# Kernel optimization log

Hardware: AMD Instinct MI355X
Metric: run time of the kernel (lower is better)

## Reference

```python
import jax, jax.numpy as jnp
import numpy as np

B, T, W = 4, 2048, 1024
K, G = 7, 8            # kernel_size, groups
Cg = W // G            # channels per group
SE_R = 16              # SE reduction ratio
LN_EPS = 1e-5


def setup_inputs() -> dict:
    key = jax.random.key(0)
    ks = jax.random.split(key, 8)
    h = jax.random.normal(ks[0], (B, T, W), jnp.float32)
    # mask: True = padding; valid prefix of random length per row
    lengths = jax.random.randint(ks[1], (B,), T // 2, T + 1)
    mask = jnp.arange(T)[None, :] >= lengths[:, None]
    s_w = np.float32(1.0 / np.sqrt(W))
    return dict(
        h=h,
        mask=mask,
        offset_w=jax.random.normal(ks[2], (W, K), jnp.float32) * 0.01,
        offset_b=jnp.zeros((K,), jnp.float32),
        conv_w=jax.random.normal(ks[3], (G, Cg, Cg, K), jnp.float32) * np.float32(1.0 / np.sqrt(Cg * K)),
        conv_b=jnp.zeros((W,), jnp.float32),
        ln_g=jnp.ones((W,), jnp.float32),
        ln_b=jnp.zeros((W,), jnp.float32),
        se_w1=jax.random.normal(ks[4], (W, W // SE_R), jnp.float32) * s_w,
        se_b1=jnp.zeros((W // SE_R,), jnp.float32),
        se_w2=jax.random.normal(ks[5], (W // SE_R, W), jnp.float32) * np.float32(1.0 / np.sqrt(W // SE_R)),
        se_b2=jnp.zeros((W,), jnp.float32),
        proj_w=jax.random.normal(ks[6], (W, 1), jnp.float32) * s_w,
        proj_b=jnp.zeros((1,), jnp.float32),
    )


def deform_conv1d(h, offset_w, offset_b, conv_w, conv_b):
    # h: [B,T,W]. Learned per-(position, tap) fractional offsets; linear interp gather;
    # grouped conv combine. conv_w: [G, out_per_group, in_per_group, K].
    Bn, Tn, Wn = h.shape
    pad = (K - 1) // 2
    offsets = h @ offset_w + offset_b                                   # [B,T,K]
    base = (jnp.arange(Tn, dtype=jnp.float32)[None, :, None]
            + (jnp.arange(K, dtype=jnp.float32) - pad)[None, None, :])  # [1,T,K]
    pos = jnp.clip(base + offsets, 0.0, Tn - 1.0)                       # [B,T,K]
    p0 = jnp.floor(pos).astype(jnp.int32)
    p1 = jnp.minimum(p0 + 1, Tn - 1)
    frac = (pos - p0.astype(jnp.float32))[..., None]                    # [B,T,K,1]
    gather = jax.vmap(lambda hb, ib: hb[ib])                            # [T,W],[T,K] -> [T,K,W]
    sampled = gather(h, p0) * (1.0 - frac) + gather(h, p1) * frac       # [B,T,K,W]
    sg = sampled.reshape(Bn, Tn, K, G, Cg)
    out = jnp.einsum('btkgc,gock->btgo', sg, conv_w).reshape(Bn, Tn, Wn)
    return out + conv_b


def layer_norm(x, g, b):
    mu = jnp.mean(x, axis=-1, keepdims=True)
    var = jnp.mean(jnp.square(x - mu), axis=-1, keepdims=True)
    return (x - mu) * jax.lax.rsqrt(var + LN_EPS) * g + b


def se_block(x, mask, w1, b1, w2, b2):
    valid = (~mask).astype(x.dtype)[..., None]                          # [B,T,1]
    lengths = jnp.clip(jnp.sum(valid, axis=1), 1.0)                     # [B,1]
    s = jnp.sum(x * valid, axis=1) / lengths                            # [B,W]
    gate = jax.nn.sigmoid(jax.nn.relu(s @ w1 + b1) @ w2 + b2)           # [B,W]
    return x * gate[:, None, :]


def reference(h, mask, offset_w, offset_b, conv_w, conv_b, ln_g, ln_b,
              se_w1, se_b1, se_w2, se_b2, proj_w, proj_b):
    x = layer_norm(deform_conv1d(h, offset_w, offset_b, conv_w, conv_b), ln_g, ln_b)
    x = se_block(x, mask, se_w1, se_b1, se_w2, se_b2)
    # dropout: identity in eval mode (p handled outside reference)
    valid = (~mask).astype(x.dtype)[..., None]
    x = x * valid                                                       # masked_fill(mask, 0)
    lengths = jnp.clip(jnp.sum(valid, axis=1), 1.0)                     # [B,1]
    pooled = jnp.sum(x, axis=1) / lengths                               # [B,W]
    return jnp.squeeze(pooled @ proj_w + proj_b, axis=-1)               # [B]
```

## Files before the change

kernel.cpp:

```cpp
#include <hip/hip_runtime.h>
#include <hip/hip_bf16.h>

#define Bdim 4
#define Tdim 2048
#define Wdim 1024
#define Kdim 7
#define Gdim 8
#define Cg   128
#define Hdim 64
#define TT   64

typedef __attribute__((ext_vector_type(8))) short short8v;
typedef __attribute__((ext_vector_type(4))) float float4v;

__device__ __forceinline__ short f2bf(float x) {
    union { float f; unsigned u; } v; v.f = x;
    unsigned r = v.u + 0x7fff + ((v.u >> 16) & 1);
    return (short)(r >> 16);
}

__device__ __forceinline__ unsigned pack2bf(float lo, float hi) {
    return __builtin_amdgcn_perm(__float_as_uint(hi) + 0x8000u,
                                 __float_as_uint(lo) + 0x8000u, 0x07060302u);
}

__device__ __forceinline__ short8v lerp_pack(uint4 a, uint4 b, float f) {
    union { uint4 u; short8v s; } r;
    const unsigned* pa = (const unsigned*)&a;
    const unsigned* pb = (const unsigned*)&b;
    unsigned* pr = (unsigned*)&r.u;
#pragma unroll
    for (int d = 0; d < 4; d++) {
        float alo = __uint_as_float(pa[d] << 16);
        float ahi = __uint_as_float(pa[d] & 0xffff0000u);
        float blo = __uint_as_float(pb[d] << 16);
        float bhi = __uint_as_float(pb[d] & 0xffff0000u);
        float rlo = alo + f * (blo - alo);
        float rhi = ahi + f * (bhi - ahi);
        pr[d] = pack2bf(rlo, rhi);
    }
    return r.s;
}

__global__ __launch_bounds__(256) void k_pre(const float* __restrict__ conv_w,
                                             short* __restrict__ Wtb,
                                             const float* __restrict__ h,
                                             const float* __restrict__ offset_w,
                                             const float* __restrict__ offset_b,
                                             float* __restrict__ pos,
                                             ushort* __restrict__ h16,
                                             float* __restrict__ rowstat) {
    int tid = threadIdx.x;
    if (blockIdx.x < 448) {
        if (blockIdx.x < 64) rowstat[blockIdx.x * 256 + tid] = 0.f;
        int i = blockIdx.x * 256 + tid;
        int cb = i & 15;
        int o = (i >> 4) & 127;
        int gk = i >> 11;
        int k = gk % Kdim, g = gk / Kdim;
        const float* src = conv_w + ((size_t)(g * Cg + o) * Cg + cb * 8) * Kdim + k;
        short8v pk;
#pragma unroll
        for (int j = 0; j < 8; j++) pk[j] = f2bf(src[(size_t)j * Kdim]);
        short8v* Wtb8 = (short8v*)Wtb;
        Wtb8[(size_t)gk * 2048 + o * 16 + cb] = pk;
        return;
    }
    int lane = tid & 63, wv = tid >> 6;
    int bt = (blockIdx.x - 448) * 4 + wv;
    int t = bt & (Tdim - 1);
    const float* row = h + (size_t)bt * Wdim;
    float acc[Kdim];
#pragma unroll
    for (int k = 0; k < Kdim; k++) acc[k] = 0.f;
#pragma unroll
    for (int j = 0; j < 4; j++) {
        int c = lane * 4 + j * 256;
        float4 hv = *(const float4*)(row + c);
        const float* ow = offset_w + (size_t)c * Kdim;
#pragma unroll
        for (int k = 0; k < Kdim; k++)
            acc[k] += hv.x * ow[k] + hv.y * ow[Kdim + k] + hv.z * ow[2 * Kdim + k]
                    + hv.w * ow[3 * Kdim + k];
        ushort4 hp;
        hp.x = (ushort)f2bf(hv.x); hp.y = (ushort)f2bf(hv.y);
        hp.z = (ushort)f2bf(hv.z); hp.w = (ushort)f2bf(hv.w);
        *(ushort4*)(h16 + (size_t)bt * Wdim + c) = hp;
    }
#pragma unroll
    for (int k = 0; k < Kdim; k++) {
#pragma unroll
        for (int m = 32; m > 0; m >>= 1) acc[k] += __shfl_xor(acc[k], m);
    }
    if (lane < Kdim) {
        float o = acc[lane] + offset_b[lane];
        float base = (float)t + (float)(lane - 3);
        float p = fminf(fmaxf(base + o, 0.f), (float)(Tdim - 1));
        pos[bt * Kdim + lane] = p;
    }
}

__global__ __launch_bounds__(256, 3) void k_conv(const ushort* __restrict__ h16,
                                                 const short* __restrict__ Wtb,
                                                 const float* __restrict__ conv_b,
                                                 const float* __restrict__ pos,
                                                 ushort* __restrict__ y16,
                                                 float* __restrict__ rowstat) {
    __shared__ short8v sA8[2][TT * 16];
    __shared__ float posl[TT * 8];

    int blk = blockIdx.x;
    int g  = blk & 7;
    int tc = (blk >> 3) & 31;
    int b  = blk >> 8;
    int t0 = tc * TT;
    int tid = threadIdx.x;
    int lane = tid & 63, wv = tid >> 6;
    int r15 = lane & 15, q = lane >> 4;

    const ushort* hb = h16 + (size_t)(b * Tdim) * Wdim + g * Cg;
    const short8v* WtbV = (const short8v*)Wtb + (size_t)(g * Kdim) * 2048;

    int scb = tid & 15;
    int sr0 = tid >> 4;

    {
        int base = (b * Tdim + t0) * Kdim;
        for (int u = tid; u < TT * Kdim; u += 256) {
            int r = u / 7, kk = u - r * 7;
            posl[r * 8 + kk] = pos[base + u];
        }
    }
    __syncthreads();

    float4v acc[4][2];
#pragma unroll
    for (int tt = 0; tt < 4; tt++)
#pragma unroll
        for (int n = 0; n < 2; n++) acc[tt][n] = (float4v){0.f, 0.f, 0.f, 0.f};

    float fr[4];
    uint4 glo[4], ghi[4];
    short8v bfr[8];

#pragma unroll
    for (int i = 0; i < 4; i++) {
        int r = sr0 + i * 16;
        float p = posl[r * 8 + 0];
        int p0 = (int)p;
        fr[i] = p - (float)p0;
        int p1 = min(p0 + 1, Tdim - 1);
        glo[i] = *(const uint4*)(hb + (size_t)p0 * Wdim + scb * 8);
        ghi[i] = *(const uint4*)(hb + (size_t)p1 * Wdim + scb * 8);
    }
#pragma unroll
    for (int n = 0; n < 2; n++)
#pragma unroll
        for (int kk = 0; kk < 4; kk++)
            bfr[n * 4 + kk] = WtbV[(wv * 32 + n * 16 + r15) * 16 + kk * 4 + q];
#pragma unroll
    for (int i = 0; i < 4; i++) {
        int r = sr0 + i * 16;
        sA8[0][r * 16 + (scb ^ (r & 7))] = lerp_pack(glo[i], ghi[i], fr[i]);
    }
    asm volatile("s_waitcnt lgkmcnt(0)" ::: "memory");
    __builtin_amdgcn_s_barrier();
    asm volatile("" ::: "memory");

#pragma unroll 1
    for (int k = 0; k < Kdim; k++) {
        int cur = k & 1;
        short8v* buf = sA8[cur];
        if (k < Kdim - 1) {
#pragma unroll
            for (int i = 0; i < 4; i++) {
                int r = sr0 + i * 16;
                float p = posl[r * 8 + k + 1];
                int p0 = (int)p;
                fr[i] = p - (float)p0;
                int p1 = min(p0 + 1, Tdim - 1);
                glo[i] = *(const uint4*)(hb + (size_t)p0 * Wdim + scb * 8);
                ghi[i] = *(const uint4*)(hb + (size_t)p1 * Wdim + scb * 8);
            }
        }
#pragma unroll
        for (int tt = 0; tt < 4; tt++) {
            int r = tt * 16 + r15;
            short8v af[4];
#pragma unroll
            for (int kk = 0; kk < 4; kk++)
                af[kk] = buf[r * 16 + ((kk * 4 + q) ^ (r & 7))];
#pragma unroll
            for (int kk = 0; kk < 4; kk++) {
#pragma unroll
                for (int n = 0; n < 2; n++)
                    acc[tt][n] = __builtin_amdgcn_mfma_f32_16x16x32_bf16(
                        af[kk], bfr[n * 4 + kk], acc[tt][n], 0, 0, 0);
            }
        }
        if (k < Kdim - 1) {
            short8v* nbuf = sA8[cur ^ 1];
#pragma unroll
            for (int i = 0; i < 4; i++) {
                int r = sr0 + i * 16;
                nbuf[r * 16 + (scb ^ (r & 7))] = lerp_pack(glo[i], ghi[i], fr[i]);
            }
#pragma unroll
            for (int n = 0; n < 2; n++)
#pragma unroll
                for (int kk = 0; kk < 4; kk++)
                    bfr[n * 4 + kk] =
                        WtbV[(size_t)(k + 1) * 2048 + (wv * 32 + n * 16 + r15) * 16 + kk * 4 + q];
            asm volatile("s_waitcnt lgkmcnt(0)" ::: "memory");
            __builtin_amdgcn_s_barrier();
            asm volatile("" ::: "memory");
        }
    }
    __syncthreads();
    float* ep = (float*)sA8;
#pragma unroll
    for (int n = 0; n < 2; n++) {
        int colb = wv * 32 + n * 16 + r15;
        float bias = conv_b[g * Cg + colb];
#pragma unroll
        for (int tt = 0; tt < 4; tt++)
#pragma unroll
            for (int j = 0; j < 4; j++) {
                int row = tt * 16 + q * 4 + j;
                ep[row * 128 + (colb ^ ((row & 7) << 2))] = acc[tt][n][j] + bias;
            }
    }
    __syncthreads();
    int row = tid >> 2, c0 = (tid & 3) * 32;
    int sw = (row & 7) << 2;
    ushort* yp = y16 + (size_t)(b * Tdim + t0 + row) * Wdim + g * Cg + c0;
    float s_part = 0.f, q_part = 0.f;
#pragma unroll
    for (int s = 0; s < 4; s++) {
        float4 va = *(const float4*)&ep[row * 128 + ((c0 + s * 8) ^ sw)];
        float4 vb = *(const float4*)&ep[row * 128 + ((c0 + s * 8 + 4) ^ sw)];
        s_part += va.x + va.y + va.z + va.w + vb.x + vb.y + vb.z + vb.w;
        q_part += va.x * va.x + va.y * va.y + va.z * va.z + va.w * va.w
                + vb.x * vb.x + vb.y * vb.y + vb.z * vb.z + vb.w * vb.w;
        uint4 o;
        o.x = pack2bf(va.x, va.y);
        o.y = pack2bf(va.z, va.w);
        o.z = pack2bf(vb.x, vb.y);
        o.w = pack2bf(vb.z, vb.w);
        *(uint4*)(yp + s * 8) = o;
    }
    s_part += __shfl_xor(s_part, 1); s_part += __shfl_xor(s_part, 2);
    q_part += __shfl_xor(q_part, 1); q_part += __shfl_xor(q_part, 2);
    if ((tid & 3) == 0) {
        atomicAdd(&rowstat[(b * Tdim + t0 + row) * 2 + 0], s_part);
        atomicAdd(&rowstat[(b * Tdim + t0 + row) * 2 + 1], q_part);
    }
}

__global__ __launch_bounds__(256) void k_lnpool(const ushort* __restrict__ y16,
                                                const int* __restrict__ mask,
                                                const float* __restrict__ rowstat,
                                                float* __restrict__ part) {
    int blk = blockIdx.x;
    int b = blk >> 7, ch = blk & 127;
    int tid = threadIdx.x;
    int c0 = tid * 4;
    float a0 = 0.f, a1 = 0.f, a2 = 0.f, a3 = 0.f;
#pragma unroll 4
    for (int i = 0; i < 16; i++) {
        int t = ch * 16 + i;
        if (mask[b * Tdim + t]) continue;
        float2 st = *(const float2*)(rowstat + (b * Tdim + t) * 2);
        float mu = st.x * (1.f / Wdim);
        float inv = rsqrtf(st.y * (1.f / Wdim) - mu * mu + 1e-5f);
        uint2 u = *(const uint2*)(y16 + (size_t)(b * Tdim + t) * Wdim + c0);
        float v0 = __uint_as_float(u.x << 16);
        float v1 = __uint_as_float(u.x & 0xffff0000u);
        float v2 = __uint_as_float(u.y << 16);
        float v3 = __uint_as_float(u.y & 0xffff0000u);
        a0 += (v0 - mu) * inv; a1 += (v1 - mu) * inv;
        a2 += (v2 - mu) * inv; a3 += (v3 - mu) * inv;
    }
    *(float4*)(part + (size_t)blk * Wdim + c0) = (float4){a0, a1, a2, a3};
}

__global__ __launch_bounds__(256) void k_sefinal(const float* __restrict__ part,
                                                 const int* __restrict__ mask,
                                                 const float* __restrict__ ln_g,
                                                 const float* __restrict__ ln_b,
                                                 const float* __restrict__ w1,
                                                 const float* __restrict__ b1,
                                                 const float* __restrict__ w2,
                                                 const float* __restrict__ b2,
                                                 const float* __restrict__ projw,
                                                 const float* __restrict__ projb,
                                                 float* __restrict__ out) {
    int b = blockIdx.x, tid = threadIdx.x;
    __shared__ float s[Wdim];
    __shared__ float hred[4][Hdim];
    __shared__ float hid[Hdim];
    __shared__ float rbuf[4];
    __shared__ float sLinv;
    int lane = tid & 63, wv = tid >> 6;

    int cnt = 0;
    for (int t = tid; t < Tdim; t += 256) cnt += (mask[b * Tdim + t] ? 0 : 1);
    float fc = (float)cnt;
#pragma unroll
    for (int off = 32; off > 0; off >>= 1) fc += __shfl_down(fc, off);
    if (lane == 0) rbuf[wv] = fc;
    __syncthreads();
    if (tid == 0) {
        float L = rbuf[0] + rbuf[1] + rbuf[2] + rbuf[3];
        sLinv = 1.f / fmaxf(L, 1.f);
    }
    __syncthreads();
    float Linv = sLinv;

    int w4 = tid * 4;
    float4 a = {0.f, 0.f, 0.f, 0.f};
    for (int chh = 0; chh < 128; chh++) {
        float4 p = *(const float4*)(part + (size_t)(b * 128 + chh) * Wdim + w4);
        a.x += p.x; a.y += p.y; a.z += p.z; a.w += p.w;
    }
    float4 gg = *(const float4*)(ln_g + w4);
    float4 bb = *(const float4*)(ln_b + w4);
    s[w4 + 0] = gg.x * (a.x * Linv) + bb.x;
    s[w4 + 1] = gg.y * (a.y * Linv) + bb.y;
    s[w4 + 2] = gg.z * (a.z * Linv) + bb.z;
    s[w4 + 3] = gg.w * (a.w * Linv) + bb.w;
    __syncthreads();

    int j = tid & 63, p = tid >> 6;
    float ha = 0.f;
    for (int w = p * 256; w < (p + 1) * 256; ++w) ha += s[w] * w1[(size_t)w * Hdim + j];
    hred[p][j] = ha;
    __syncthreads();
    if (tid < Hdim)
        hid[tid] = fmaxf(hred[0][tid] + hred[1][tid] + hred[2][tid] + hred[3][tid] + b1[tid], 0.f);
    __syncthreads();

    float part2 = 0.f;
    for (int w = tid; w < Wdim; w += 256) {
        float ga = b2[w];
#pragma unroll 8
        for (int j2 = 0; j2 < Hdim; j2++) ga += hid[j2] * w2[(size_t)j2 * Wdim + w];
        float gate = 1.f / (1.f + expf(-ga));
        part2 += s[w] * gate * projw[w];
    }
#pragma unroll
    for (int off = 32; off > 0; off >>= 1) part2 += __shfl_down(part2, off);
    __syncthreads();
    if (lane == 0) rbuf[wv] = part2;
    __syncthreads();
    if (tid == 0) out[b] = rbuf[0] + rbuf[1] + rbuf[2] + rbuf[3] + projb[0];
}

extern "C" void kernel_launch(void* const* d_in, const int* in_sizes, int n_in,
                              void* d_out, int out_size, void* d_ws, size_t ws_size,
                              hipStream_t stream) {
    const float* h        = (const float*)d_in[0];
    const int*   mask     = (const int*)d_in[1];
    const float* offset_w = (const float*)d_in[2];
    const float* offset_b = (const float*)d_in[3];
    const float* conv_w   = (const float*)d_in[4];
    const float* conv_b   = (const float*)d_in[5];
    const float* ln_g     = (const float*)d_in[6];
    const float* ln_b     = (const float*)d_in[7];
    const float* se_w1    = (const float*)d_in[8];
    const float* se_b1    = (const float*)d_in[9];
    const float* se_w2    = (const float*)d_in[10];
    const float* se_b2    = (const float*)d_in[11];
    const float* proj_w   = (const float*)d_in[12];
    const float* proj_b   = (const float*)d_in[13];
    float* out = (float*)d_out;

    char* wsb = (char*)d_ws;
    float*  pos     = (float*)(wsb);
    ushort* h16     = (ushort*)(wsb + 229376);
    short*  Wtb     = (short*)(wsb + 17006592);
    ushort* y16     = (ushort*)(wsb + 18841600);
    float*  rowstat = (float*)(wsb + 35618816);
    float*  part    = (float*)(wsb + 35684352);

    k_pre<<<dim3(448 + Bdim * Tdim / 4), dim3(256), 0, stream>>>(conv_w, Wtb, h, offset_w,
                                                                 offset_b, pos, h16, rowstat);
    k_conv<<<dim3(Bdim * (Tdim / TT) * Gdim), dim3(256), 0, stream>>>(h16, Wtb, conv_b,
                                                                      pos, y16, rowstat);
    k_lnpool<<<dim3(Bdim * 128), dim3(256), 0, stream>>>(y16, mask, rowstat, part);
    k_sefinal<<<dim3(Bdim), dim3(256), 0, stream>>>(part, mask, ln_g, ln_b,
                                                    se_w1, se_b1, se_w2, se_b2,
                                                    proj_w, proj_b, out);
}
```

Measured before the change: 110.0 us.

## Prefetch all deform-conv taps into LDS upfront with smaller time tiles

The grouped deformable conv kernel now handles 32 time rows per block instead of 64. Each thread issues all seven taps' interpolation gathers at the start and writes the lerped bf16 rows for every tap into one LDS buffer. This replaces the per-tap double-buffered gather with a barrier on every tap, so the MFMA loop over taps runs with no block synchronisation and only software-prefetches weights in registers. In exchange, LDS use and register pressure go up (launch bound relaxed to 2 blocks/CU), and each block does less MFMA work to amortise the weight loads.

```diff
diff --git a/kernel.cpp b/kernel.cpp
--- a/kernel.cpp
+++ b/kernel.cpp
@@ -8,7 +8,7 @@
 #define Gdim 8
 #define Cg   128
 #define Hdim 64
-#define TT   64
+#define TT   32
 
 typedef __attribute__((ext_vector_type(8))) short short8v;
 typedef __attribute__((ext_vector_type(4))) float float4v;
@@ -100,19 +100,18 @@
     }
 }
 
-__global__ __launch_bounds__(256, 3) void k_conv(const ushort* __restrict__ h16,
+__global__ __launch_bounds__(256, 2) void k_conv(const ushort* __restrict__ h16,
                                                  const short* __restrict__ Wtb,
                                                  const float* __restrict__ conv_b,
                                                  const float* __restrict__ pos,
                                                  ushort* __restrict__ y16,
                                                  float* __restrict__ rowstat) {
-    __shared__ short8v sA8[2][TT * 16];
-    __shared__ float posl[TT * 8];
+    __shared__ short8v sA[TT * Kdim * 16];
 
     int blk = blockIdx.x;
     int g  = blk & 7;
-    int tc = (blk >> 3) & 31;
-    int b  = blk >> 8;
+    int tc = (blk >> 3) & 63;
+    int b  = blk >> 9;
     int t0 = tc * TT;
     int tid = threadIdx.x;
     int lane = tid & 63, wv = tid >> 6;
@@ -122,136 +121,118 @@
     const short8v* WtbV = (const short8v*)Wtb + (size_t)(g * Kdim) * 2048;
 
     int scb = tid & 15;
-    int sr0 = tid >> 4;
-
-    {
-        int base = (b * Tdim + t0) * Kdim;
-        for (int u = tid; u < TT * Kdim; u += 256) {
-            int r = u / 7, kk = u - r * 7;
-            posl[r * 8 + kk] = pos[base + u];
+    int srow = tid >> 4;
+
+    float fr[2][Kdim];
+    uint4 glo[2][Kdim], ghi[2][Kdim];
+#pragma unroll
+    for (int hf = 0; hf < 2; hf++) {
+        int r = srow + hf * 16;
+        int rbase = (b * Tdim + t0 + r) * Kdim;
+#pragma unroll
+        for (int k = 0; k < Kdim; k++) {
+            float p = pos[rbase + k];
+            int p0 = (int)p;
+            fr[hf][k] = p - (float)p0;
+            int p1 = min(p0 + 1, Tdim - 1);
+            glo[hf][k] = *(const uint4*)(hb + (size_t)p0 * Wdim + scb * 8);
+            ghi[hf][k] = *(const uint4*)(hb + (size_t)p1 * Wdim + scb * 8);
         }
     }
-    __syncthreads();
-
-    float4v acc[4][2];
-#pragma unroll
-    for (int tt = 0; tt < 4; tt++)
-#pragma unroll
-        for (int n = 0; n < 2; n++) acc[tt][n] = (float4v){0.f, 0.f, 0.f, 0.f};
-
-    float fr[4];
-    uint4 glo[4], ghi[4];
-    short8v bfr[8];
-
-#pragma unroll
-    for (int i = 0; i < 4; i++) {
-        int r = sr0 + i * 16;
-        float p = posl[r * 8 + 0];
-        int p0 = (int)p;
-        fr[i] = p - (float)p0;
-        int p1 = min(p0 + 1, Tdim - 1);
-        glo[i] = *(const uint4*)(hb + (size_t)p0 * Wdim + scb * 8);
-        ghi[i] = *(const uint4*)(hb + (size_t)p1 * Wdim + scb * 8);
-    }
-#pragma unroll
-    for (int n = 0; n < 2; n++)
-#pragma unroll
-        for (int kk = 0; kk < 4; kk++)
-            bfr[n * 4 + kk] = WtbV[(wv * 32 + n * 16 + r15) * 16 + kk * 4 + q];
-#pragma unroll
-    for (int i = 0; i < 4; i++) {
-        int r = sr0 + i * 16;
-        sA8[0][r * 16 + (scb ^ (r & 7))] = lerp_pack(glo[i], ghi[i], fr[i]);
-    }
-    asm volatile("s_waitcnt lgkmcnt(0)" ::: "memory");
-    __builtin_amdgcn_s_barrier();
-    asm volatile("" ::: "memory");
-
-#pragma unroll 1
+#pragma unroll
+    for (int hf = 0; hf < 2; hf++) {
+        int r = srow + hf * 16;
+#pragma unroll
+        for (int k = 0; k < Kdim; k++)
+            sA[(r * Kdim + k) * 16 + (scb ^ (r & 7))] =
+                lerp_pack(glo[hf][k], ghi[hf][k], fr[hf][k]);
+    }
+    __syncthreads();
+
+    float4v acc[2][2];
+#pragma unroll
+    for (int ts = 0; ts < 2; ts++)
+#pragma unroll
+        for (int os = 0; os < 2; os++) acc[ts][os] = (float4v){0.f, 0.f, 0.f, 0.f};
+
+    short8v bcur[8];
+#pragma unroll
+    for (int j = 0; j < 8; j++) {
+        int os = j >> 2, kk = j & 3;
+        bcur[j] = WtbV[(wv * 32 + os * 16 + r15) * 16 + kk * 4 + q];
+    }
+#pragma unroll
     for (int k = 0; k < Kdim; k++) {
-        int cur = k & 1;
-        short8v* buf = sA8[cur];
+        short8v bnext[8];
         if (k < Kdim - 1) {
 #pragma unroll
-            for (int i = 0; i < 4; i++) {
-                int r = sr0 + i * 16;
-                float p = posl[r * 8 + k + 1];
-                int p0 = (int)p;
-                fr[i] = p - (float)p0;
-                int p1 = min(p0 + 1, Tdim - 1);
-                glo[i] = *(const uint4*)(hb + (size_t)p0 * Wdim + scb * 8);
-                ghi[i] = *(const uint4*)(hb + (size_t)p1 * Wdim + scb * 8);
+            for (int j = 0; j < 8; j++) {
+                int os = j >> 2, kk = j & 3;
+                bnext[j] = WtbV[(size_t)(k + 1) * 2048 + (wv * 32 + os * 16 + r15) * 16 + kk * 4 + q];
             }
         }
-#pragma unroll
-        for (int tt = 0; tt < 4; tt++) {
-            int r = tt * 16 + r15;
-            short8v af[4];
+        short8v af[2][4];
+#pragma unroll
+        for (int ts = 0; ts < 2; ts++) {
+            int r = ts * 16 + r15;
 #pragma unroll
             for (int kk = 0; kk < 4; kk++)
-                af[kk] = buf[r * 16 + ((kk * 4 + q) ^ (r & 7))];
-#pragma unroll
-            for (int kk = 0; kk < 4; kk++) {
-#pragma unroll
-                for (int n = 0; n < 2; n++)
-                    acc[tt][n] = __builtin_amdgcn_mfma_f32_16x16x32_bf16(
-                        af[kk], bfr[n * 4 + kk], acc[tt][n], 0, 0, 0);
+                af[ts][kk] = sA[(r * Kdim + k) * 16 + ((kk * 4 + q) ^ (r15 & 7))];
+        }
+#pragma unroll
+        for (int kk = 0; kk < 4; kk++)
+#pragma unroll
+            for (int ts = 0; ts < 2; ts++)
+#pragma unroll
+                for (int os = 0; os < 2; os++)
+                    acc[ts][os] = __builtin_amdgcn_mfma_f32_16x16x32_bf16(
+                        af[ts][kk], bcur[os * 4 + kk], acc[ts][os], 0, 0, 0);
+        if (k < Kdim - 1) {
+#pragma unroll
+            for (int j = 0; j < 8; j++) bcur[j] = bnext[j];
+        }
+    }
+
+    __syncthreads();
+    float* ep = (float*)sA;
+#pragma unroll
+    for (int os = 0; os < 2; os++) {
+        int colb = wv * 32 + os * 16 + r15;
+        float bias = conv_b[g * Cg + colb];
+#pragma unroll
+        for (int ts = 0; ts < 2; ts++)
+#pragma unroll
+            for (int j = 0; j < 4; j++) {
+                int row = ts * 16 + q * 4 + j;
+                ep[row * 128 + (colb ^ ((row & 7) << 2))] = acc[ts][os][j] + bias;
             }
-        }
-        if (k < Kdim - 1) {
-            short8v* nbuf = sA8[cur ^ 1];
-#pragma unroll
-            for (int i = 0; i < 4; i++) {
-                int r = sr0 + i * 16;
-                nbuf[r * 16 + (scb ^ (r & 7))] = lerp_pack(glo[i], ghi[i], fr[i]);
-            }
-#pragma unroll
-            for (int n = 0; n < 2; n++)
-#pragma unroll
-                for (int kk = 0; kk < 4; kk++)
-                    bfr[n * 4 + kk] =
-                        WtbV[(size_t)(k + 1) * 2048 + (wv * 32 + n * 16 + r15) * 16 + kk * 4 + q];
-            asm volatile("s_waitcnt lgkmcnt(0)" ::: "memory");
-            __builtin_amdgcn_s_barrier();
-            asm volatile("" ::: "memory");
-        }
-    }
-    __syncthreads();
-    float* ep = (float*)sA8;
-#pragma unroll
-    for (int n = 0; n < 2; n++) {
-        int colb = wv * 32 + n * 16 + r15;
-        float bias = conv_b[g * Cg + colb];
-#pragma unroll
-        for (int tt = 0; tt < 4; tt++)
-#pragma unroll
-            for (int j = 0; j < 4; j++) {
-                int row = tt * 16 + q * 4 + j;
-                ep[row * 128 + (colb ^ ((row & 7) << 2))] = acc[tt][n][j] + bias;
-            }
-    }
-    __syncthreads();
-    int row = tid >> 2, c0 = (tid & 3) * 32;
+    }
+    __syncthreads();
+    int row = tid >> 3, c0 = (tid & 7) * 16;
     int sw = (row & 7) << 2;
+    float4 v0 = *(const float4*)&ep[row * 128 + ((c0 + 0) ^ sw)];
+    float4 v1 = *(const float4*)&ep[row * 128 + ((c0 + 4) ^ sw)];
+    float4 v2 = *(const float4*)&ep[row * 128 + ((c0 + 8) ^ sw)];
+    float4 v3 = *(const float4*)&ep[row * 128 + ((c0 + 12) ^ sw)];
     ushort* yp = y16 + (size_t)(b * Tdim + t0 + row) * Wdim + g * Cg + c0;
-    float s_part = 0.f, q_part = 0.f;
-#pragma unroll
-    for (int s = 0; s < 4; s++) {
-        float4 va = *(const float4*)&ep[row * 128 + ((c0 + s * 8) ^ sw)];
-        float4 vb = *(const float4*)&ep[row * 128 + ((c0 + s * 8 + 4) ^ sw)];
-        s_part += va.x + va.y + va.z + va.w + vb.x + vb.y + vb.z + vb.w;
-        q_part += va.x * va.x + va.y * va.y + va.z * va.z + va.w * va.w
-                + vb.x * vb.x + vb.y * vb.y + vb.z * vb.z + vb.w * vb.w;
-        uint4 o;
-        o.x = pack2bf(va.x, va.y);
-        o.y = pack2bf(va.z, va.w);
-        o.z = pack2bf(vb.x, vb.y);
-        o.w = pack2bf(vb.z, vb.w);
-        *(uint4*)(yp + s * 8) = o;
-    }
+    uint4 o0, o1;
+    o0.x = pack2bf(v0.x, v0.y); o0.y = pack2bf(v0.z, v0.w);
+    o0.z = pack2bf(v1.x, v1.y); o0.w = pack2bf(v1.z, v1.w);
+    o1.x = pack2bf(v2.x, v2.y); o1.y = pack2bf(v2.z, v2.w);
+    o1.z = pack2bf(v3.x, v3.y); o1.w = pack2bf(v3.z, v3.w);
+    *(uint4*)yp = o0;
+    *(uint4*)(yp + 8) = o1;
+    float s_part = v0.x + v0.y + v0.z + v0.w + v1.x + v1.y + v1.z + v1.w
+                 + v2.x + v2.y + v2.z + v2.w + v3.x + v3.y + v3.z + v3.w;
+    float q_part = v0.x * v0.x + v0.y * v0.y + v0.z * v0.z + v0.w * v0.w
+                 + v1.x * v1.x + v1.y * v1.y + v1.z * v1.z + v1.w * v1.w
+                 + v2.x * v2.x + v2.y * v2.y + v2.z * v2.z + v2.w * v2.w
+                 + v3.x * v3.x + v3.y * v3.y + v3.z * v3.z + v3.w * v3.w;
     s_part += __shfl_xor(s_part, 1); s_part += __shfl_xor(s_part, 2);
+    s_part += __shfl_xor(s_part, 4);
     q_part += __shfl_xor(q_part, 1); q_part += __shfl_xor(q_part, 2);
-    if ((tid & 3) == 0) {
+    q_part += __shfl_xor(q_part, 4);
+    if ((tid & 7) == 0) {
         atomicAdd(&rowstat[(b * Tdim + t0 + row) * 2 + 0], s_part);
         atomicAdd(&rowstat[(b * Tdim + t0 + row) * 2 + 1], q_part);
     }
```

Result: slower. 128.7 us (+17.1%).
